# Optimization experiments

Hardware: AMD Instinct MI355X
Metric: run time of the kernel (lower is better)

The kernel has to match this reference:

```python
import jax, jax.numpy as jnp
import numpy as np

EPS = 1e-7      # geometric epsilon used in LOAI_features
BN_EPS = 1e-5   # torch BatchNorm default eps (eval mode)
B, N, C = 8, 8192, 2
S, K = 1024, 32
C_PREV = 64


def _index_points(points, idx):
    # points [B,N,C], idx [B,S,K] int -> [B,S,K,C] (torch index_points)
    return jax.vmap(lambda p, i: p[i])(points, idx)


def _conv_bn_relu(x, w, b, g, beta, m, v):
    # 1x1 Conv2d + eval-mode BatchNorm2d + ReLU. x [B,Cin,K,S], w [Cout,Cin]
    y = jnp.einsum('bcks,oc->boks', x, w) + b[None, :, None, None]
    scale = g * jax.lax.rsqrt(v + BN_EPS)
    y = (y - m[None, :, None, None]) * scale[None, :, None, None] + beta[None, :, None, None]
    return jax.nn.relu(y)


def setup_inputs() -> dict:
    key = jax.random.key(0)
    ks = jax.random.split(key, 8)
    contour = jax.random.normal(ks[0], (B, N, C), jnp.float32)
    loa = jax.random.normal(ks[1], (B, N, C), jnp.float32)
    loa = loa / (jnp.linalg.norm(loa, axis=-1, keepdims=True) + 1e-8)  # unit LOA vectors
    prev = jax.random.normal(ks[2], (B, C_PREV, N), jnp.float32)

    def lin(k, o, i):
        return jax.random.normal(k, (o, i), jnp.float32) * (1.0 / np.sqrt(i))

    d = {
        'contour_all_points': contour,
        'LOA_all_points': loa,
        'feature_maps_from_prev_layer': prev,
        # feature-enhancement MLP: 8 -> 32 -> 64
        'ew1': lin(ks[3], 32, 8), 'eb1': jnp.zeros(32), 'eg1': jnp.ones(32),
        'ebeta1': jnp.zeros(32), 'em1': jnp.zeros(32), 'ev1': jnp.ones(32),
        'ew2': lin(ks[4], 64, 32), 'eb2': jnp.zeros(64), 'eg2': jnp.ones(64),
        'ebeta2': jnp.zeros(64), 'em2': jnp.zeros(64), 'ev2': jnp.ones(64),
        # filter MLP: (64 + C_PREV)=128 -> 128 -> 256
        'fw1': lin(ks[5], 128, 64 + C_PREV), 'fb1': jnp.zeros(128), 'fg1': jnp.ones(128),
        'fbeta1': jnp.zeros(128), 'fm1': jnp.zeros(128), 'fv1': jnp.ones(128),
        'fw2': lin(ks[6], 256, 128), 'fb2': jnp.zeros(256), 'fg2': jnp.ones(256),
        'fbeta2': jnp.zeros(256), 'fm2': jnp.zeros(256), 'fv2': jnp.ones(256),
    }
    return d


def reference(contour_all_points, LOA_all_points, feature_maps_from_prev_layer,
              ew1, eb1, eg1, ebeta1, em1, ev1,
              ew2, eb2, eg2, ebeta2, em2, ev2,
              fw1, fb1, fg1, fbeta1, fm1, fv1,
              fw2, fb2, fg2, fbeta2, fm2, fv2):
    # --- downsampling: linspace indices over contour (static) ---
    new_idx = np.linspace(0, N - 1, S).astype(np.int64)              # [S]
    gidx_np = (new_idx[None, :, None] - K // 2 + np.arange(K)[None, None, :]) % N  # [1,S,K]
    gidx = jnp.broadcast_to(jnp.asarray(gidx_np), (B, S, K))

    sampled = contour_all_points[:, new_idx, :]                      # [B,S,C]
    loa_ci = LOA_all_points[:, new_idx, :][:, :, None, :]            # [B,S,1,C]

    # --- gather neighbor windows ---
    xi = _index_points(contour_all_points, gidx)                     # [B,S,K,C]
    loa_xi = _index_points(LOA_all_points, gidx)                     # [B,S,K,C]

    def sdot(a, b):
        return jnp.sum(a * b, axis=-1, keepdims=True)

    def oriented_angle(cos_a, cos_b, dotp):
        ang = jnp.arccos(jnp.clip(dotp, -1.0 + EPS, 1.0 - EPS))
        sign = jnp.where(cos_a < cos_b, 1.0, -1.0)  # equal case -> -1, as in torch
        return sign * ang

    # --- rotation-invariant features ---
    vec = xi - sampled[:, :, None, :]
    f4 = jnp.linalg.norm(vec, axis=-1, keepdims=True)                # dist ci->xi
    u = vec / (f4 + EPS)
    a1 = sdot(loa_ci, u)
    a2 = sdot(loa_xi, -u)
    f3o = oriented_angle(a1, a2, sdot(loa_xi, loa_ci))

    vecp = xi - jnp.roll(xi, 1, axis=2)
    vecp = vecp.at[:, :, 0, :].set(0.0)
    f8 = jnp.linalg.norm(vecp, axis=-1, keepdims=True)
    up = vecp / (f8 + EPS)
    loa_xim1 = jnp.roll(loa_xi, 1, axis=2).at[:, :, 0, :].set(0.0)
    a4 = sdot(up, loa_xi)
    a5 = sdot(up, loa_xim1)
    f7o = oriented_angle(a4, a5, sdot(loa_xi, loa_xim1))

    ru = jnp.roll(u, 1, axis=2).at[:, :, 0, :].set(0.0)
    d2 = jnp.arccos(jnp.clip(sdot(u, ru), -1.0 + EPS, 1.0 - EPS))

    rif = jnp.concatenate([f4, d2, a1, a2, f3o, a4, a5, f7o], axis=-1)  # [B,S,K,8]

    # --- feature enhancement MLP on [B,8,K,S] ---
    x = jnp.transpose(rif, (0, 3, 2, 1))
    x = _conv_bn_relu(x, ew1, eb1, eg1, ebeta1, em1, ev1)
    x = _conv_bn_relu(x, ew2, eb2, eg2, ebeta2, em2, ev2)            # [B,64,K,S]

    # --- group previous-layer features and concat ---
    prev_bnc = jnp.transpose(feature_maps_from_prev_layer, (0, 2, 1))  # [B,N,Cp]
    grouped_prev = _index_points(prev_bnc, gidx)                     # [B,S,K,Cp]
    grouped_prev = jnp.transpose(grouped_prev, (0, 3, 2, 1))         # [B,Cp,K,S]
    x = jnp.concatenate([x, grouped_prev], axis=1)                   # [B,128,K,S]

    # --- filter MLP + max-pool over neighbors ---
    x = _conv_bn_relu(x, fw1, fb1, fg1, fbeta1, fm1, fv1)
    x = _conv_bn_relu(x, fw2, fb2, fg2, fbeta2, fm2, fv2)            # [B,256,K,S]
    out = jnp.max(x, axis=2)                                         # [B,256,S]
    return out
```

## Files before the change

kernel.cpp:

```cpp
#include <hip/hip_runtime.h>
#include <math.h>

namespace {

constexpr int Nn = 8192;
constexpr int Ss = 1024;
constexpr float F_EPS = 1e-7f;
constexpr float F_BN_EPS = 1e-5f;

typedef __attribute__((ext_vector_type(8))) short s16x8;
typedef __attribute__((ext_vector_type(4))) float f32x4;

constexpr int WB3 = 0;
constexpr int WB4 = 32768;
constexpr int BB3 = 98304;
constexpr int BB4 = 98816;
constexpr int EW1 = 99840;
constexpr int EB1 = 100864;
constexpr int EW2 = 100992;
constexpr int EB2 = 109184;
constexpr size_t WS_NEED = 109440;

constexpr size_t CATO = 131072;
constexpr size_t WS_BIG = CATO + 33554432ull;

__device__ inline unsigned short f2bf(float f) {
  unsigned int u = __builtin_bit_cast(unsigned int, f);
  u += 0x7fffu + ((u >> 16) & 1u);
  return (unsigned short)(u >> 16);
}

__device__ inline s16x8 pack_scaled(const float* __restrict__ p, float sc) {
  const float4 w0 = *(const float4*)p;
  const float4 w1 = *(const float4*)(p + 4);
  s16x8 r;
  r[0] = (short)f2bf(w0.x * sc); r[1] = (short)f2bf(w0.y * sc);
  r[2] = (short)f2bf(w0.z * sc); r[3] = (short)f2bf(w0.w * sc);
  r[4] = (short)f2bf(w1.x * sc); r[5] = (short)f2bf(w1.y * sc);
  r[6] = (short)f2bf(w1.z * sc); r[7] = (short)f2bf(w1.w * sc);
  return r;
}

__device__ inline s16x8 prev_frag(const float* __restrict__ prev, int b, int cbase, int n) {
  const float* p = prev + (size_t)(b * 64 + cbase) * Nn + n;
  s16x8 r;
#pragma unroll
  for (int j = 0; j < 8; ++j) r[j] = (short)f2bf(p[j * Nn]);
  return r;
}

__device__ inline int ci_of(int s) {
  return (s == Ss - 1) ? (Nn - 1) : (int)(long long)((double)s * (8191.0 / 1023.0));
}

__global__ __launch_bounds__(256) void rcri_prep(
    const float* __restrict__ ew1, const float* __restrict__ eb1,
    const float* __restrict__ eg1, const float* __restrict__ ebeta1,
    const float* __restrict__ em1, const float* __restrict__ ev1,
    const float* __restrict__ ew2, const float* __restrict__ eb2,
    const float* __restrict__ eg2, const float* __restrict__ ebeta2,
    const float* __restrict__ em2, const float* __restrict__ ev2,
    const float* __restrict__ fw1, const float* __restrict__ fb1,
    const float* __restrict__ fg1, const float* __restrict__ fbeta1,
    const float* __restrict__ fm1, const float* __restrict__ fv1,
    const float* __restrict__ fw2, const float* __restrict__ fb2,
    const float* __restrict__ fg2, const float* __restrict__ fbeta2,
    const float* __restrict__ fm2, const float* __restrict__ fv2,
    unsigned char* __restrict__ ws)
{
  const int i = blockIdx.x * 256 + threadIdx.x;
  if (i < 16384) {
    const int o = i >> 7;
    const float sc = fg1[o] * rsqrtf(fv1[o] + F_BN_EPS);
    ((unsigned short*)(ws + WB3))[i] = f2bf(fw1[i] * sc);
    return;
  }
  int j = i - 16384;
  if (j < 32768) {
    const int o = j >> 7;
    const float sc = fg2[o] * rsqrtf(fv2[o] + F_BN_EPS);
    ((unsigned short*)(ws + WB4))[j] = f2bf(fw2[j] * sc);
    return;
  }
  j -= 32768;
  if (j < 128) {
    const float sc = fg1[j] * rsqrtf(fv1[j] + F_BN_EPS);
    ((float*)(ws + BB3))[j] = (fb1[j] - fm1[j]) * sc + fbeta1[j];
    return;
  }
  j -= 128;
  if (j < 256) {
    const float sc = fg2[j] * rsqrtf(fv2[j] + F_BN_EPS);
    ((float*)(ws + BB4))[j] = (fb2[j] - fm2[j]) * sc + fbeta2[j];
    return;
  }
  j -= 256;
  if (j < 256) {
    const int o = j >> 3;
    const float sc = eg1[o] * rsqrtf(ev1[o] + F_BN_EPS);
    ((float*)(ws + EW1))[j] = ew1[j] * sc;
    return;
  }
  j -= 256;
  if (j < 32) {
    const float sc = eg1[j] * rsqrtf(ev1[j] + F_BN_EPS);
    ((float*)(ws + EB1))[j] = (eb1[j] - em1[j]) * sc + ebeta1[j];
    return;
  }
  j -= 32;
  if (j < 2048) {
    const int o = j >> 5;
    const float sc = eg2[o] * rsqrtf(ev2[o] + F_BN_EPS);
    ((float*)(ws + EW2))[j] = ew2[j] * sc;
    return;
  }
  j -= 2048;
  if (j < 64) {
    const float sc = eg2[j] * rsqrtf(ev2[j] + F_BN_EPS);
    ((float*)(ws + EB2))[j] = (eb2[j] - em2[j]) * sc + ebeta2[j];
  }
}

__global__ __launch_bounds__(256) void rcri_k1f(
    const float* __restrict__ contour, const float* __restrict__ loa,
    unsigned char* __restrict__ ws)
{
  __shared__ float wlds[2400];
  __shared__ __align__(16) unsigned char cstage[256 * 144];

  const int t = threadIdx.x;
  for (int j = t; j < 2400; j += 256) wlds[j] = ((const float*)(ws + EW1))[j];

  const int row = blockIdx.x * 256 + t;
  const int b = row >> 15;
  const int s = (row >> 5) & 1023;
  const int kk = row & 31;
  const int ci = ci_of(s);
  const int n = (ci - 16 + kk) & (Nn - 1);

  const float2* c2 = (const float2*)contour;
  const float2* l2 = (const float2*)loa;

  const float2 xi = c2[b * Nn + n];
  const float2 lx = l2[b * Nn + n];
  const float2 sp = c2[b * Nn + ci];
  const float2 lc = l2[b * Nn + ci];

  float2 xim1 = make_float2(0.f, 0.f), lxm1 = make_float2(0.f, 0.f);
  if (kk > 0) {
    const int np = (ci - 16 + kk - 1) & (Nn - 1);
    xim1 = c2[b * Nn + np];
    lxm1 = l2[b * Nn + np];
  }

  const float vx = xi.x - sp.x, vy = xi.y - sp.y;
  const float f4 = sqrtf(vx * vx + vy * vy);
  const float inv = 1.0f / (f4 + F_EPS);
  const float ux = vx * inv, uy = vy * inv;
  const float a1 = lc.x * ux + lc.y * uy;
  const float a2 = -(lx.x * ux + lx.y * uy);
  float dotp = lx.x * lc.x + lx.y * lc.y;
  float cl = fminf(fmaxf(dotp, -1.0f + F_EPS), 1.0f - F_EPS);
  const float f3o = (a1 < a2 ? 1.0f : -1.0f) * acosf(cl);

  float pux = 0.f, puy = 0.f;
  if (kk > 0) {
    const float pvx = xim1.x - sp.x, pvy = xim1.y - sp.y;
    const float pf4 = sqrtf(pvx * pvx + pvy * pvy);
    const float pinv = 1.0f / (pf4 + F_EPS);
    pux = pvx * pinv; puy = pvy * pinv;
  }
  const float vpx = (kk > 0) ? (xi.x - xim1.x) : 0.0f;
  const float vpy = (kk > 0) ? (xi.y - xim1.y) : 0.0f;
  const float f8 = sqrtf(vpx * vpx + vpy * vpy);
  const float invp = 1.0f / (f8 + F_EPS);
  const float upx = vpx * invp, upy = vpy * invp;
  const float a4 = upx * lx.x + upy * lx.y;
  const float a5 = upx * lxm1.x + upy * lxm1.y;
  float dotp2 = lx.x * lxm1.x + lx.y * lxm1.y;
  float cl2 = fminf(fmaxf(dotp2, -1.0f + F_EPS), 1.0f - F_EPS);
  const float f7o = (a4 < a5 ? 1.0f : -1.0f) * acosf(cl2);
  float du = ux * pux + uy * puy;
  float cl3 = fminf(fmaxf(du, -1.0f + F_EPS), 1.0f - F_EPS);
  const float d2 = acosf(cl3);

  __syncthreads();

  float h1v[32];
#pragma unroll
  for (int o = 0; o < 32; ++o) {
    const float4 w0 = *(const float4*)(wlds + o * 8);
    const float4 w1 = *(const float4*)(wlds + o * 8 + 4);
    float acc = wlds[256 + o]
      + w0.x * f4  + w0.y * d2  + w0.z * a1  + w0.w * a2
      + w1.x * f3o + w1.y * a4  + w1.z * a5  + w1.w * f7o;
    h1v[o] = fmaxf(acc, 0.f);
  }

#pragma unroll
  for (int grp = 0; grp < 8; ++grp) {
    unsigned int uu[4];
#pragma unroll
    for (int q = 0; q < 4; ++q) {
      float y2[2];
#pragma unroll
      for (int jj = 0; jj < 2; ++jj) {
        const int o = grp * 8 + q * 2 + jj;
        float acc = wlds[2336 + o];
#pragma unroll
        for (int c4 = 0; c4 < 8; ++c4) {
          const float4 ww = *(const float4*)(wlds + 288 + o * 32 + c4 * 4);
          acc += ww.x * h1v[c4 * 4 + 0] + ww.y * h1v[c4 * 4 + 1]
               + ww.z * h1v[c4 * 4 + 2] + ww.w * h1v[c4 * 4 + 3];
        }
        y2[jj] = fmaxf(acc, 0.f);
      }
      uu[q] = (unsigned)f2bf(y2[0]) | ((unsigned)f2bf(y2[1]) << 16);
    }
    *(uint4*)(cstage + t * 144 + grp * 16) = make_uint4(uu[0], uu[1], uu[2], uu[3]);
  }
  __syncthreads();

#pragma unroll
  for (int it = 0; it < 8; ++it) {
    const int idx = it * 256 + t;
    const int rr = idx >> 3;
    const int cc = idx & 7;
    const uint4 v = *(const uint4*)(cstage + rr * 144 + cc * 16);
    *(uint4*)(ws + CATO + (size_t)(blockIdx.x * 256 + rr) * 128 + cc * 16) = v;
  }
}

__global__ __launch_bounds__(256) void rcri_k23(
    const float* __restrict__ prev, const unsigned char* __restrict__ ws,
    float* __restrict__ out)
{
  __shared__ __align__(16) unsigned char h3s[65536];
  __shared__ float obuf[256 * 9];

  const int t = threadIdx.x;
  const int lane = t & 63;
  const int w = t >> 6;
  const int rl = lane & 15;
  const int g = lane >> 4;
  const int rows0 = blockIdx.x * 256;
  const int b = blockIdx.x >> 7;
  const int sbase = (blockIdx.x & 127) * 8;

  {
    const unsigned short* wb3 = (const unsigned short*)(ws + WB3);
    const float* b3p = (const float*)(ws + BB3);
    s16x8 B3[2][4];
    float bb3[2];
#pragma unroll
    for (int i = 0; i < 2; ++i) {
      const int o = (2 * w + i) * 16 + rl;
#pragma unroll
      for (int kt = 0; kt < 4; ++kt)
        B3[i][kt] = *(const s16x8*)(wb3 + o * 128 + kt * 32 + 8 * g);
      bb3[i] = b3p[o];
    }
    for (int mt = 0; mt < 16; ++mt) {
      const int row = rows0 + mt * 16 + rl;
      const int s = (row >> 5) & 1023;
      const int kk = row & 31;
      const int ci = ci_of(s);
      const int n = (ci - 16 + kk) & (Nn - 1);

      const s16x8 a0 = __builtin_bit_cast(s16x8,
          *(const uint4*)(ws + CATO + (size_t)row * 128 + 16 * g));
      const s16x8 a1 = __builtin_bit_cast(s16x8,
          *(const uint4*)(ws + CATO + (size_t)row * 128 + 64 + 16 * g));
      const s16x8 a2 = prev_frag(prev, b, 8 * g, n);
      const s16x8 a3 = prev_frag(prev, b, 32 + 8 * g, n);

#pragma unroll
      for (int i = 0; i < 2; ++i) {
        f32x4 acc = {0.f, 0.f, 0.f, 0.f};
        acc = __builtin_amdgcn_mfma_f32_16x16x32_bf16(a0, B3[i][0], acc, 0, 0, 0);
        acc = __builtin_amdgcn_mfma_f32_16x16x32_bf16(a1, B3[i][1], acc, 0, 0, 0);
        acc = __builtin_amdgcn_mfma_f32_16x16x32_bf16(a2, B3[i][2], acc, 0, 0, 0);
        acc = __builtin_amdgcn_mfma_f32_16x16x32_bf16(a3, B3[i][3], acc, 0, 0, 0);
        const int o = (2 * w + i) * 16 + rl;
#pragma unroll
        for (int r = 0; r < 4; ++r) {
          const int row2 = mt * 16 + 4 * g + r;
          const float y = fmaxf(acc[r] + bb3[i], 0.f);
          *(unsigned short*)(h3s + row2 * 256 + ((2 * o) ^ ((row2 & 15) << 4))) = f2bf(y);
        }
      }
    }
  }
  __syncthreads();

  {
    const unsigned short* wb4 = (const unsigned short*)(ws + WB4);
    const float* b4p = (const float*)(ws + BB4);
    s16x8 B4[4][4];
    float bb4[4];
#pragma unroll
    for (int ni = 0; ni < 4; ++ni) {
      const int o = (4 * w + ni) * 16 + rl;
#pragma unroll
      for (int kt = 0; kt < 4; ++kt)
        B4[ni][kt] = *(const s16x8*)(wb4 + o * 128 + kt * 32 + 8 * g);
      bb4[ni] = b4p[o];
    }
    float vmax[4] = {-INFINITY, -INFINITY, -INFINITY, -INFINITY};
    for (int mt = 0; mt < 16; ++mt) {
      const int rowl = mt * 16 + rl;
      s16x8 a[4];
#pragma unroll
      for (int kt = 0; kt < 4; ++kt)
        a[kt] = __builtin_bit_cast(s16x8,
            *(const uint4*)(h3s + rowl * 256 + ((kt * 64 + 16 * g) ^ ((rowl & 15) << 4))));
#pragma unroll
      for (int ni = 0; ni < 4; ++ni) {
        f32x4 acc = {0.f, 0.f, 0.f, 0.f};
        acc = __builtin_amdgcn_mfma_f32_16x16x32_bf16(a[0], B4[ni][0], acc, 0, 0, 0);
        acc = __builtin_amdgcn_mfma_f32_16x16x32_bf16(a[1], B4[ni][1], acc, 0, 0, 0);
        acc = __builtin_amdgcn_mfma_f32_16x16x32_bf16(a[2], B4[ni][2], acc, 0, 0, 0);
        acc = __builtin_amdgcn_mfma_f32_16x16x32_bf16(a[3], B4[ni][3], acc, 0, 0, 0);
#pragma unroll
        for (int r = 0; r < 4; ++r)
          vmax[ni] = fmaxf(vmax[ni], fmaxf(acc[r] + bb4[ni], 0.f));
      }
      if (mt & 1) {
        const int sl = mt >> 1;
#pragma unroll
        for (int ni = 0; ni < 4; ++ni) {
          float v = vmax[ni];
          v = fmaxf(v, __shfl_xor(v, 16));
          v = fmaxf(v, __shfl_xor(v, 32));
          if (g == 0) {
            const int o = (4 * w + ni) * 16 + rl;
            obuf[o * 9 + sl] = v;
          }
          vmax[ni] = -INFINITY;
        }
      }
    }
  }
  __syncthreads();
  {
    float v[8];
#pragma unroll
    for (int j = 0; j < 8; ++j) v[j] = obuf[t * 9 + j];
    float* po = out + ((size_t)(b * 256 + t) << 10) + sbase;
    float4 v0; v0.x = v[0]; v0.y = v[1]; v0.z = v[2]; v0.w = v[3];
    float4 v1; v1.x = v[4]; v1.y = v[5]; v1.z = v[6]; v1.w = v[7];
    *(float4*)po = v0;
    *(float4*)(po + 4) = v1;
  }
}

template <bool P>
__global__ __launch_bounds__(256, 2) void rcri_main(
    const float* __restrict__ contour, const float* __restrict__ loa,
    const float* __restrict__ prev, const unsigned char* __restrict__ ws,
    const float* __restrict__ ew1, const float* __restrict__ eb1,
    const float* __restrict__ eg1, const float* __restrict__ ebeta1,
    const float* __restrict__ em1, const float* __restrict__ ev1,
    const float* __restrict__ ew2, const float* __restrict__ eb2,
    const float* __restrict__ eg2, const float* __restrict__ ebeta2,
    const float* __restrict__ em2, const float* __restrict__ ev2,
    const float* __restrict__ fw1, const float* __restrict__ fb1,
    const float* __restrict__ fg1, const float* __restrict__ fbeta1,
    const float* __restrict__ fm1, const float* __restrict__ fv1,
    const float* __restrict__ fw2, const float* __restrict__ fb2,
    const float* __restrict__ fg2, const float* __restrict__ fbeta2,
    const float* __restrict__ fm2, const float* __restrict__ fv2,
    float* __restrict__ out)
{
  __shared__ __align__(16) unsigned char smem[65536 + 9216];
  float* obuf = (float*)(smem + 65536);

  const int t = threadIdx.x;
  const int lane = t & 63;
  const int w = t >> 6;
  const int rl = lane & 15;
  const int g = lane >> 4;
  const int blk = blockIdx.x;
  const int b = blk >> 7;
  const int s_base = (blk & 127) << 3;

  const unsigned short* wb3 = (const unsigned short*)(ws + WB3);
  const unsigned short* wb4 = (const unsigned short*)(ws + WB4);
  const float* b3p = (const float*)(ws + BB3);
  const float* b4p = (const float*)(ws + BB4);
  const float* w1p = (const float*)(ws + EW1);
  const float* b1p = (const float*)(ws + EB1);
  const float* w2p = (const float*)(ws + EW2);
  const float* b2p = (const float*)(ws + EB2);

  const float2* c2 = (const float2*)contour;
  const float2* l2 = (const float2*)loa;

  auto cat_off = [](int m, int byte) { return m * 256 + (byte ^ ((m & 15) << 4)); };
  auto h3_off  = [](int m, int byte) { return 32768 + m * 256 + (byte ^ ((m & 15) << 4)); };

  for (int hh = 0; hh < 2; ++hh) {
    {
      const int m = t & 127;
      const int hf = t >> 7;
      const int sl4 = m >> 5, kk = m & 31;
      const int s = s_base + hh * 4 + sl4;
      const int ci = ci_of(s);
      const int n = (ci - 16 + kk) & (Nn - 1);

#pragma unroll
      for (int u = 0; u < 8; ++u) {
        const int c0 = hf * 32 + u * 4;
        const float* pp = prev + (size_t)(b * 64 + c0) * Nn + n;
        const float p0 = pp[0], p1 = pp[Nn], p2 = pp[2 * Nn], p3 = pp[3 * Nn];
        const unsigned int u0 = (unsigned)f2bf(p0) | ((unsigned)f2bf(p1) << 16);
        const unsigned int u1 = (unsigned)f2bf(p2) | ((unsigned)f2bf(p3) << 16);
        *(uint2*)(smem + cat_off(m, 128 + 2 * c0)) = make_uint2(u0, u1);
      }

      const float2 xi = c2[b * Nn + n];
      const float2 lx = l2[b * Nn + n];
      const float2 sp = c2[b * Nn + ci];
      const float2 lc = l2[b * Nn + ci];

      float2 xim1 = make_float2(0.f, 0.f), lxm1 = make_float2(0.f, 0.f);
      if (kk > 0) {
        const int np = (ci - 16 + kk - 1) & (Nn - 1);
        xim1 = c2[b * Nn + np];
        lxm1 = l2[b * Nn + np];
      }

      const float vx = xi.x - sp.x, vy = xi.y - sp.y;
      const float f4 = sqrtf(vx * vx + vy * vy);
      const float inv = 1.0f / (f4 + F_EPS);
      const float ux = vx * inv, uy = vy * inv;
      const float a1 = lc.x * ux + lc.y * uy;
      const float a2 = -(lx.x * ux + lx.y * uy);
      float dotp = lx.x * lc.x + lx.y * lc.y;
      float cl = fminf(fmaxf(dotp, -1.0f + F_EPS), 1.0f - F_EPS);
      const float f3o = (a1 < a2 ? 1.0f : -1.0f) * acosf(cl);

      float pux = 0.f, puy = 0.f;
      if (kk > 0) {
        const float pvx = xim1.x - sp.x, pvy = xim1.y - sp.y;
        const float pf4 = sqrtf(pvx * pvx + pvy * pvy);
        const float pinv = 1.0f / (pf4 + F_EPS);
        pux = pvx * pinv; puy = pvy * pinv;
      }
      const float vpx = (kk > 0) ? (xi.x - xim1.x) : 0.0f;
      const float vpy = (kk > 0) ? (xi.y - xim1.y) : 0.0f;
      const float f8 = sqrtf(vpx * vpx + vpy * vpy);
      const float invp = 1.0f / (f8 + F_EPS);
      const float upx = vpx * invp, upy = vpy * invp;
      const float a4 = upx * lx.x + upy * lx.y;
      const float a5 = upx * lxm1.x + upy * lxm1.y;
      float dotp2 = lx.x * lxm1.x + lx.y * lxm1.y;
      float cl2 = fminf(fmaxf(dotp2, -1.0f + F_EPS), 1.0f - F_EPS);
      const float f7o = (a4 < a5 ? 1.0f : -1.0f) * acosf(cl2);
      float du = ux * pux + uy * puy;
      float cl3 = fminf(fmaxf(du, -1.0f + F_EPS), 1.0f - F_EPS);
      const float d2 = acosf(cl3);

      const float rif[8] = {f4, d2, a1, a2, f3o, a4, a5, f7o};

      float h1v[32];
#pragma unroll
      for (int o = 0; o < 32; ++o) {
        float acc;
        if (P) {
          acc = b1p[o];
#pragma unroll
          for (int c = 0; c < 8; ++c) acc += w1p[o * 8 + c] * rif[c];
        } else {
          float a0 = 0.f;
#pragma unroll
          for (int c = 0; c < 8; ++c) a0 += ew1[o * 8 + c] * rif[c];
          const float sc = eg1[o] * rsqrtf(ev1[o] + F_BN_EPS);
          acc = (a0 + eb1[o] - em1[o]) * sc + ebeta1[o];
        }
        h1v[o] = fmaxf(acc, 0.f);
      }

#pragma unroll
      for (int i = 0; i < 8; ++i) {
        float yv[4];
#pragma unroll
        for (int j = 0; j < 4; ++j) {
          const int o = hf * 32 + i * 4 + j;
          float acc;
          if (P) {
            acc = b2p[o];
#pragma unroll
            for (int c = 0; c < 32; ++c) acc += w2p[o * 32 + c] * h1v[c];
          } else {
            float a0 = 0.f;
#pragma unroll
            for (int c = 0; c < 32; ++c) a0 += ew2[o * 32 + c] * h1v[c];
            const float sc = eg2[o] * rsqrtf(ev2[o] + F_BN_EPS);
            acc = (a0 + eb2[o] - em2[o]) * sc + ebeta2[o];
          }
          yv[j] = fmaxf(acc, 0.f);
        }
        const unsigned int u0 = (unsigned)f2bf(yv[0]) | ((unsigned)f2bf(yv[1]) << 16);
        const unsigned int u1 = (unsigned)f2bf(yv[2]) | ((unsigned)f2bf(yv[3]) << 16);
        *(uint2*)(smem + cat_off(m, 64 * hf + 8 * i)) = make_uint2(u0, u1);
      }
    }
    __syncthreads();

    {
      s16x8 B3[2][4];
      float bb3[2];
#pragma unroll
      for (int i = 0; i < 2; ++i) {
        const int o = (2 * w + i) * 16 + rl;
        if (P) {
#pragma unroll
          for (int kt = 0; kt < 4; ++kt)
            B3[i][kt] = *(const s16x8*)(wb3 + o * 128 + kt * 32 + 8 * g);
          bb3[i] = b3p[o];
        } else {
          const float sc = fg1[o] * rsqrtf(fv1[o] + F_BN_EPS);
#pragma unroll
          for (int kt = 0; kt < 4; ++kt)
            B3[i][kt] = pack_scaled(fw1 + o * 128 + kt * 32 + 8 * g, sc);
          bb3[i] = (fb1[o] - fm1[o]) * sc + fbeta1[o];
        }
      }
      for (int mt = 0; mt < 8; ++mt) {
        const int row = mt * 16 + rl;
        s16x8 a[4];
#pragma unroll
        for (int kt = 0; kt < 4; ++kt)
          a[kt] = __builtin_bit_cast(s16x8, *(const uint4*)(smem + cat_off(row, kt * 64 + 16 * g)));
#pragma unroll
        for (int i = 0; i < 2; ++i) {
          f32x4 acc = {0.f, 0.f, 0.f, 0.f};
          acc = __builtin_amdgcn_mfma_f32_16x16x32_bf16(a[0], B3[i][0], acc, 0, 0, 0);
          acc = __builtin_amdgcn_mfma_f32_16x16x32_bf16(a[1], B3[i][1], acc, 0, 0, 0);
          acc = __builtin_amdgcn_mfma_f32_16x16x32_bf16(a[2], B3[i][2], acc, 0, 0, 0);
          acc = __builtin_amdgcn_mfma_f32_16x16x32_bf16(a[3], B3[i][3], acc, 0, 0, 0);
          const int o = (2 * w + i) * 16 + rl;
#pragma unroll
          for (int r = 0; r < 4; ++r) {
            const float y = fmaxf(acc[r] + bb3[i], 0.f);
            *(unsigned short*)(smem + h3_off(mt * 16 + 4 * g + r, 2 * o)) = f2bf(y);
          }
        }
      }
    }
    __syncthreads();

#pragma unroll
    for (int nip = 0; nip < 2; ++nip) {
      s16x8 B4[2][4];
      float bb4[2];
#pragma unroll
      for (int q = 0; q < 2; ++q) {
        const int o = (4 * w + nip * 2 + q) * 16 + rl;
        if (P) {
#pragma unroll
          for (int kt = 0; kt < 4; ++kt)
            B4[q][kt] = *(const s16x8*)(wb4 + o * 128 + kt * 32 + 8 * g);
          bb4[q] = b4p[o];
        } else {
          const float sc = fg2[o] * rsqrtf(fv2[o] + F_BN_EPS);
#pragma unroll
          for (int kt = 0; kt < 4; ++kt)
            B4[q][kt] = pack_scaled(fw2 + o * 128 + kt * 32 + 8 * g, sc);
          bb4[q] = (fb2[o] - fm2[o]) * sc + fbeta2[o];
        }
      }
      float vm[2] = {-INFINITY, -INFINITY};
      for (int mt = 0; mt < 8; ++mt) {
        const int row = mt * 16 + rl;
        s16x8 a[4];
#pragma unroll
        for (int kt = 0; kt < 4; ++kt)
          a[kt] = __builtin_bit_cast(s16x8, *(const uint4*)(smem + h3_off(row, kt * 64 + 16 * g)));
#pragma unroll
        for (int q = 0; q < 2; ++q) {
          f32x4 acc = {0.f, 0.f, 0.f, 0.f};
          acc = __builtin_amdgcn_mfma_f32_16x16x32_bf16(a[0], B4[q][0], acc, 0, 0, 0);
          acc = __builtin_amdgcn_mfma_f32_16x16x32_bf16(a[1], B4[q][1], acc, 0, 0, 0);
          acc = __builtin_amdgcn_mfma_f32_16x16x32_bf16(a[2], B4[q][2], acc, 0, 0, 0);
          acc = __builtin_amdgcn_mfma_f32_16x16x32_bf16(a[3], B4[q][3], acc, 0, 0, 0);
#pragma unroll
          for (int r = 0; r < 4; ++r)
            vm[q] = fmaxf(vm[q], fmaxf(acc[r] + bb4[q], 0.f));
        }
        if (mt & 1) {
          const int sl = hh * 4 + (mt >> 1);
#pragma unroll
          for (int q = 0; q < 2; ++q) {
            float v = vm[q];
            v = fmaxf(v, __shfl_xor(v, 16));
            v = fmaxf(v, __shfl_xor(v, 32));
            if (g == 0) {
              const int o = (4 * w + nip * 2 + q) * 16 + rl;
              obuf[o * 9 + sl] = v;
            }
            vm[q] = -INFINITY;
          }
        }
      }
    }
  }

  __syncthreads();
  {
    float v[8];
#pragma unroll
    for (int j = 0; j < 8; ++j) v[j] = obuf[t * 9 + j];
    float* po = out + ((size_t)(b * 256 + t) << 10) + s_base;
    float4 v0; v0.x = v[0]; v0.y = v[1]; v0.z = v[2]; v0.w = v[3];
    float4 v1; v1.x = v[4]; v1.y = v[5]; v1.z = v[6]; v1.w = v[7];
    *(float4*)po = v0;
    *(float4*)(po + 4) = v1;
  }
}

}

extern "C" void kernel_launch(void* const* d_in, const int* in_sizes, int n_in,
                              void* d_out, int out_size, void* d_ws, size_t ws_size,
                              hipStream_t stream) {
  (void)in_sizes; (void)n_in; (void)out_size;

  const float* contour = (const float*)d_in[0];
  const float* loa     = (const float*)d_in[1];
  const float* prev    = (const float*)d_in[2];
  const float* ew1 = (const float*)d_in[3];
  const float* eb1 = (const float*)d_in[4];
  const float* eg1 = (const float*)d_in[5];
  const float* ebeta1 = (const float*)d_in[6];
  const float* em1 = (const float*)d_in[7];
  const float* ev1 = (const float*)d_in[8];
  const float* ew2 = (const float*)d_in[9];
  const float* eb2 = (const float*)d_in[10];
  const float* eg2 = (const float*)d_in[11];
  const float* ebeta2 = (const float*)d_in[12];
  const float* em2 = (const float*)d_in[13];
  const float* ev2 = (const float*)d_in[14];
  const float* fw1 = (const float*)d_in[15];
  const float* fb1 = (const float*)d_in[16];
  const float* fg1 = (const float*)d_in[17];
  const float* fbeta1 = (const float*)d_in[18];
  const float* fm1 = (const float*)d_in[19];
  const float* fv1 = (const float*)d_in[20];
  const float* fw2 = (const float*)d_in[21];
  const float* fb2 = (const float*)d_in[22];
  const float* fg2 = (const float*)d_in[23];
  const float* fbeta2 = (const float*)d_in[24];
  const float* fm2 = (const float*)d_in[25];
  const float* fv2 = (const float*)d_in[26];

  float* out = (float*)d_out;
  unsigned char* ws = (unsigned char*)d_ws;

  if (ws && ws_size >= WS_BIG) {
    rcri_prep<<<dim3(203), dim3(256), 0, stream>>>(
        ew1, eb1, eg1, ebeta1, em1, ev1, ew2, eb2, eg2, ebeta2, em2, ev2,
        fw1, fb1, fg1, fbeta1, fm1, fv1, fw2, fb2, fg2, fbeta2, fm2, fv2, ws);
    rcri_k1f<<<dim3(1024), dim3(256), 0, stream>>>(contour, loa, ws);
    rcri_k23<<<dim3(1024), dim3(256), 0, stream>>>(prev, ws, out);
  } else if (ws && ws_size >= WS_NEED) {
    rcri_prep<<<dim3(203), dim3(256), 0, stream>>>(
        ew1, eb1, eg1, ebeta1, em1, ev1, ew2, eb2, eg2, ebeta2, em2, ev2,
        fw1, fb1, fg1, fbeta1, fm1, fv1, fw2, fb2, fg2, fbeta2, fm2, fv2, ws);
    rcri_main<true><<<dim3(1024), dim3(256), 0, stream>>>(
        contour, loa, prev, ws,
        ew1, eb1, eg1, ebeta1, em1, ev1, ew2, eb2, eg2, ebeta2, em2, ev2,
        fw1, fb1, fg1, fbeta1, fm1, fv1, fw2, fb2, fg2, fbeta2, fm2, fv2, out);
  } else {
    rcri_main<false><<<dim3(1024), dim3(256), 0, stream>>>(
        contour, loa, prev, ws,
        ew1, eb1, eg1, ebeta1, em1, ev1, ew2, eb2, eg2, ebeta2, em2, ev2,
        fw1, fb1, fg1, fbeta1, fm1, fv1, fw2, fb2, fg2, fbeta2, fm2, fv2, out);
  }
}
```

Baseline: 106.3 us.

## Pre-transpose prev features to bf16 rows; halve per-block rows in k1f and k23

Adds a kernel that transposes the previous-layer features into a point-major bf16 layout in workspace, so the fused MLP kernel can fetch each neighbour's 64 channels with two 16-byte loads instead of strided gathers. The k1f stage now splits each row's second-layer output channels across two threads (128 rows per block), and k23 handles 128 rows per block with half the shared memory. This doubles grid sizes and is meant to raise occupancy. The cost is one extra launch and an extra 8 MB workspace pass.

```diff
diff --git a/kernel.cpp b/kernel.cpp
--- a/kernel.cpp
+++ b/kernel.cpp
@@ -22,7 +22,8 @@
 constexpr size_t WS_NEED = 109440;
 
 constexpr size_t CATO = 131072;
-constexpr size_t WS_BIG = CATO + 33554432ull;
+constexpr size_t PVT  = CATO + 33554432ull;
+constexpr size_t WS_BIG = PVT + 8388608ull;
 
 __device__ inline unsigned short f2bf(float f) {
   unsigned int u = __builtin_bit_cast(unsigned int, f);
@@ -121,17 +122,47 @@
   }
 }
 
-__global__ __launch_bounds__(256) void rcri_k1f(
+__global__ __launch_bounds__(256) void rcri_tpose(
+    const float* __restrict__ prev, unsigned char* __restrict__ ws)
+{
+  __shared__ unsigned short tile[128 * 72];
+  const int t = threadIdx.x;
+  const int b = blockIdx.x >> 6;
+  const int n0 = (blockIdx.x & 63) * 128;
+  const int nloc = t & 127;
+  const int chalf = t >> 7;
+
+#pragma unroll
+  for (int it = 0; it < 32; ++it) {
+    const int c = it * 2 + chalf;
+    const float v = prev[(size_t)(b * 64 + c) * Nn + n0 + nloc];
+    tile[nloc * 72 + c] = f2bf(v);
+  }
+  __syncthreads();
+
+#pragma unroll
+  for (int it = 0; it < 4; ++it) {
+    const int idx = it * 256 + t;
+    const int rn = idx >> 3;
+    const int cc = idx & 7;
+    const uint4 v = *(const uint4*)((const unsigned char*)tile + rn * 144 + cc * 16);
+    *(uint4*)(ws + PVT + (size_t)(b * Nn + n0 + rn) * 128 + cc * 16) = v;
+  }
+}
+
+__global__ __launch_bounds__(256) void rcri_k1f2(
     const float* __restrict__ contour, const float* __restrict__ loa,
     unsigned char* __restrict__ ws)
 {
   __shared__ float wlds[2400];
-  __shared__ __align__(16) unsigned char cstage[256 * 144];
+  __shared__ __align__(16) unsigned char cstage[128 * 144];
 
   const int t = threadIdx.x;
   for (int j = t; j < 2400; j += 256) wlds[j] = ((const float*)(ws + EW1))[j];
 
-  const int row = blockIdx.x * 256 + t;
+  const int r = t & 127;
+  const int hf = t >> 7;
+  const int row = blockIdx.x * 128 + r;
   const int b = row >> 15;
   const int s = (row >> 5) & 1023;
   const int kk = row & 31;
@@ -198,14 +229,14 @@
   }
 
 #pragma unroll
-  for (int grp = 0; grp < 8; ++grp) {
+  for (int grp = 0; grp < 4; ++grp) {
     unsigned int uu[4];
 #pragma unroll
     for (int q = 0; q < 4; ++q) {
       float y2[2];
 #pragma unroll
       for (int jj = 0; jj < 2; ++jj) {
-        const int o = grp * 8 + q * 2 + jj;
+        const int o = hf * 32 + grp * 8 + q * 2 + jj;
         float acc = wlds[2336 + o];
 #pragma unroll
         for (int c4 = 0; c4 < 8; ++c4) {
@@ -217,35 +248,34 @@
       }
       uu[q] = (unsigned)f2bf(y2[0]) | ((unsigned)f2bf(y2[1]) << 16);
     }
-    *(uint4*)(cstage + t * 144 + grp * 16) = make_uint4(uu[0], uu[1], uu[2], uu[3]);
+    *(uint4*)(cstage + r * 144 + hf * 64 + grp * 16) = make_uint4(uu[0], uu[1], uu[2], uu[3]);
   }
   __syncthreads();
 
 #pragma unroll
-  for (int it = 0; it < 8; ++it) {
+  for (int it = 0; it < 4; ++it) {
     const int idx = it * 256 + t;
     const int rr = idx >> 3;
     const int cc = idx & 7;
     const uint4 v = *(const uint4*)(cstage + rr * 144 + cc * 16);
-    *(uint4*)(ws + CATO + (size_t)(blockIdx.x * 256 + rr) * 128 + cc * 16) = v;
+    *(uint4*)(ws + CATO + (size_t)(blockIdx.x * 128 + rr) * 128 + cc * 16) = v;
   }
 }
 
 __global__ __launch_bounds__(256) void rcri_k23(
-    const float* __restrict__ prev, const unsigned char* __restrict__ ws,
-    float* __restrict__ out)
+    const unsigned char* __restrict__ ws, float* __restrict__ out)
 {
-  __shared__ __align__(16) unsigned char h3s[65536];
-  __shared__ float obuf[256 * 9];
+  __shared__ __align__(16) unsigned char h3s[32768];
+  __shared__ float obuf[256 * 5];
 
   const int t = threadIdx.x;
   const int lane = t & 63;
   const int w = t >> 6;
   const int rl = lane & 15;
   const int g = lane >> 4;
-  const int rows0 = blockIdx.x * 256;
-  const int b = blockIdx.x >> 7;
-  const int sbase = (blockIdx.x & 127) * 8;
+  const int rows0 = blockIdx.x * 128;
+  const int b = blockIdx.x >> 8;
+  const int sbase = (blockIdx.x & 255) * 4;
 
   {
     const unsigned short* wb3 = (const unsigned short*)(ws + WB3);
@@ -260,7 +290,7 @@
         B3[i][kt] = *(const s16x8*)(wb3 + o * 128 + kt * 32 + 8 * g);
       bb3[i] = b3p[o];
     }
-    for (int mt = 0; mt < 16; ++mt) {
+    for (int mt = 0; mt < 8; ++mt) {
       const int row = rows0 + mt * 16 + rl;
       const int s = (row >> 5) & 1023;
       const int kk = row & 31;
@@ -271,8 +301,10 @@
           *(const uint4*)(ws + CATO + (size_t)row * 128 + 16 * g));
       const s16x8 a1 = __builtin_bit_cast(s16x8,
           *(const uint4*)(ws + CATO + (size_t)row * 128 + 64 + 16 * g));
-      const s16x8 a2 = prev_frag(prev, b, 8 * g, n);
-      const s16x8 a3 = prev_frag(prev, b, 32 + 8 * g, n);
+      const s16x8 a2 = __builtin_bit_cast(s16x8,
+          *(const uint4*)(ws + PVT + (size_t)(b * Nn + n) * 128 + 16 * g));
+      const s16x8 a3 = __builtin_bit_cast(s16x8,
+          *(const uint4*)(ws + PVT + (size_t)(b * Nn + n) * 128 + 64 + 16 * g));
 
 #pragma unroll
       for (int i = 0; i < 2; ++i) {
@@ -307,7 +339,7 @@
       bb4[ni] = b4p[o];
     }
     float vmax[4] = {-INFINITY, -INFINITY, -INFINITY, -INFINITY};
-    for (int mt = 0; mt < 16; ++mt) {
+    for (int mt = 0; mt < 8; ++mt) {
       const int rowl = mt * 16 + rl;
       s16x8 a[4];
 #pragma unroll
@@ -334,7 +366,7 @@
           v = fmaxf(v, __shfl_xor(v, 32));
           if (g == 0) {
             const int o = (4 * w + ni) * 16 + rl;
-            obuf[o * 9 + sl] = v;
+            obuf[o * 5 + sl] = v;
           }
           vmax[ni] = -INFINITY;
         }
@@ -343,14 +375,12 @@
   }
   __syncthreads();
   {
-    float v[8];
-#pragma unroll
-    for (int j = 0; j < 8; ++j) v[j] = obuf[t * 9 + j];
+    float v[4];
+#pragma unroll
+    for (int j = 0; j < 4; ++j) v[j] = obuf[t * 5 + j];
     float* po = out + ((size_t)(b * 256 + t) << 10) + sbase;
     float4 v0; v0.x = v[0]; v0.y = v[1]; v0.z = v[2]; v0.w = v[3];
-    float4 v1; v1.x = v[4]; v1.y = v[5]; v1.z = v[6]; v1.w = v[7];
     *(float4*)po = v0;
-    *(float4*)(po + 4) = v1;
   }
 }
 
@@ -662,8 +692,9 @@
     rcri_prep<<<dim3(203), dim3(256), 0, stream>>>(
         ew1, eb1, eg1, ebeta1, em1, ev1, ew2, eb2, eg2, ebeta2, em2, ev2,
         fw1, fb1, fg1, fbeta1, fm1, fv1, fw2, fb2, fg2, fbeta2, fm2, fv2, ws);
-    rcri_k1f<<<dim3(1024), dim3(256), 0, stream>>>(contour, loa, ws);
-    rcri_k23<<<dim3(1024), dim3(256), 0, stream>>>(prev, ws, out);
+    rcri_tpose<<<dim3(512), dim3(256), 0, stream>>>(prev, ws);
+    rcri_k1f2<<<dim3(2048), dim3(256), 0, stream>>>(contour, loa, ws);
+    rcri_k23<<<dim3(2048), dim3(256), 0, stream>>>(ws, out);
   } else if (ws && ws_size >= WS_NEED) {
     rcri_prep<<<dim3(203), dim3(256), 0, stream>>>(
         ew1, eb1, eg1, ebeta1, em1, ev1, ew2, eb2, eg2, ebeta2, em2, ev2,
```

Measured after the change: 109.5 us. +3.0%, slower.
